# Performance work log

Hardware: AMD Instinct MI355X
Metric: run time of the kernel (lower is better)

The kernel has to match this reference:

```python
import jax, jax.numpy as jnp
import numpy as np

B, T, D, H, NL = 8, 1024, 512, 8, 3
WS = (3, 5, 7)


def _mha(q_in, k_in, v_in, wq, bq, wk, bk, wv, bv, wo, bo):
    """Faithful copy of the torch MultiHeadAttention, including the
    transpose-free .view(B*H, -1, dh) head split (row-major reshape)."""
    bs = q_in.shape[0]
    dh = D // H
    q = (q_in @ wq + bq).reshape(bs * H, -1, dh)
    k = (k_in @ wk + bk).reshape(bs * H, -1, dh)
    v = (v_in @ wv + bv).reshape(bs * H, -1, dh)
    scores = jnp.einsum('bqd,bkd->bqk', q, k) / (dh ** 0.5)
    weights = jax.nn.softmax(scores, axis=-1)
    att = jnp.einsum('bqk,bkd->bqd', weights, v).reshape(bs, -1, D)
    return att @ wo + bo


def _forward(x, loc_wq, loc_bq, loc_wk, loc_bk, loc_wv, loc_bv, loc_wo, loc_bo,
             g_wq, g_bq, g_wk, g_bk, g_wv, g_bv, g_wo, g_bo, out_w, out_b):
    feats = []
    for lv in range(NL):
        w = WS[lv]
        pad = (w - 1) // 2
        xp = jnp.pad(x, ((0, 0), (pad, pad), (0, 0)))  # [B, T+2p, D]
        idx = jnp.arange(T)[:, None] + jnp.arange(w)[None, :]  # [T, w]
        win = xp[:, idx, :].reshape(B * T, w, D)  # sliding windows, same as unfold+permute
        lo = _mha(win, win, win,
                  loc_wq[lv], loc_bq[lv], loc_wk[lv], loc_bk[lv],
                  loc_wv[lv], loc_bv[lv], loc_wo[lv], loc_bo[lv])
        feats.append(lo.reshape(B, T, w, D).mean(axis=2))
    feats.append(_mha(x, x, x, g_wq, g_bq, g_wk, g_bk, g_wv, g_bv, g_wo, g_bo))
    combined = jnp.concatenate(feats, axis=-1)  # [B, T, D*(NL+1)]
    return combined @ out_w + out_b  # dropout is identity in eval mode


def setup_inputs() -> dict:
    key = jax.random.key(0)
    ks = jax.random.split(key, 20)
    s = 0.02
    d = {}
    d['x'] = jax.random.normal(ks[0], (B, T, D), jnp.float32)
    d['loc_wq'] = jax.random.normal(ks[1], (NL, D, D), jnp.float32) * s
    d['loc_bq'] = jax.random.normal(ks[2], (NL, D), jnp.float32) * s
    d['loc_wk'] = jax.random.normal(ks[3], (NL, D, D), jnp.float32) * s
    d['loc_bk'] = jax.random.normal(ks[4], (NL, D), jnp.float32) * s
    d['loc_wv'] = jax.random.normal(ks[5], (NL, D, D), jnp.float32) * s
    d['loc_bv'] = jax.random.normal(ks[6], (NL, D), jnp.float32) * s
    d['loc_wo'] = jax.random.normal(ks[7], (NL, D, D), jnp.float32) * s
    d['loc_bo'] = jax.random.normal(ks[8], (NL, D), jnp.float32) * s
    d['g_wq'] = jax.random.normal(ks[9], (D, D), jnp.float32) * s
    d['g_bq'] = jax.random.normal(ks[10], (D,), jnp.float32) * s
    d['g_wk'] = jax.random.normal(ks[11], (D, D), jnp.float32) * s
    d['g_bk'] = jax.random.normal(ks[12], (D,), jnp.float32) * s
    d['g_wv'] = jax.random.normal(ks[13], (D, D), jnp.float32) * s
    d['g_bv'] = jax.random.normal(ks[14], (D,), jnp.float32) * s
    d['g_wo'] = jax.random.normal(ks[15], (D, D), jnp.float32) * s
    d['g_bo'] = jax.random.normal(ks[16], (D,), jnp.float32) * s
    d['out_w'] = jax.random.normal(ks[17], (D * (NL + 1), D), jnp.float32) * s
    d['out_b'] = jax.random.normal(ks[18], (D,), jnp.float32) * s
    return d


def reference(x, loc_wq, loc_bq, loc_wk, loc_bk, loc_wv, loc_bv, loc_wo, loc_bo,
              g_wq, g_bq, g_wk, g_bk, g_wv, g_bv, g_wo, g_bo, out_w, out_b):
    return _forward(x, loc_wq, loc_bq, loc_wk, loc_bk, loc_wv, loc_bv, loc_wo, loc_bo,
                    g_wq, g_bq, g_wk, g_bk, g_wv, g_bv, g_wo, g_bo, out_w, out_b)
```

## Files before the change

kernel.cpp:

```cpp
#include <hip/hip_runtime.h>
#include <hip/hip_bf16.h>
#include <cstddef>

#define T_SEQ 1024
#define D_MODEL 512

typedef __attribute__((ext_vector_type(8))) __bf16 bf16x8;
typedef __attribute__((ext_vector_type(4))) float f32x4;
typedef __attribute__((ext_vector_type(16))) float f32x16;
typedef __attribute__((ext_vector_type(8))) unsigned short u16x8;
typedef __attribute__((ext_vector_type(4))) unsigned int u32x4;

typedef const unsigned int __attribute__((address_space(1)))* gas1_t;
typedef unsigned int __attribute__((address_space(3)))* las3_t;

__device__ __forceinline__ void gload_lds16(const void* g, void* l) {
  __builtin_amdgcn_global_load_lds((gas1_t)g, (las3_t)l, 16, 0, 0);
}

__device__ __forceinline__ float bf2f(unsigned short u) {
  return __uint_as_float(((unsigned)u) << 16);
}
__device__ __forceinline__ unsigned short f2bf(float f) {
  __hip_bfloat16 h = __float2bfloat16(f);
// ... 31 lines not shown
    const int base = blockIdx.x * 16384 + t * 8;
#pragma unroll
    for (int it = 0; it < 8; ++it) {
      const int i = base + it * 2048;
      const float4 a = *(const float4*)(x + i);
      const float4 b = *(const float4*)(x + i + 4);
      u16x8 o;
      o[0] = f2bf(a.x); o[1] = f2bf(a.y); o[2] = f2bf(a.z); o[3] = f2bf(a.w);
      o[4] = f2bf(b.x); o[5] = f2bf(b.y); o[6] = f2bf(b.z); o[7] = f2bf(b.w);
      *(u16x8*)(xb + i) = o;
    }
    return;
  }
  if (z == 21) {
    const int i = blockIdx.x * 256 + t;
    if (blockIdx.x < 18) {
      const int which = i >> 9, lv = which / 3, role = which % 3, e = i & 511;
      const float* src = role == 0 ? loc_bq : role == 1 ? loc_bk : loc_bv;
      bqkvb[i] = __float2bfloat16(src[lv * 512 + e]);
    }
    return;
  }

  const float* src;
  bool tr = true;
  if (z < 3)       src = loc_wq + (size_t)z * MS;
  else if (z < 6)  src = loc_wk + (size_t)(z - 3) * MS;
  else if (z < 9)  src = loc_wv + (size_t)(z - 6) * MS;
  else if (z == 9)  src = g_wq;
  else if (z == 10) src = g_wk;
  else if (z == 11) src = g_wv;
  else if (z < 16) src = out_w + (size_t)(z - 12) * MS;
  else if (z < 19) { src = loc_wo + (size_t)(z - 16) * MS; tr = false; }
  else             { src = g_wo; tr = false; }
  __hip_bfloat16* dst = WT + (size_t)z * MS;

  const int tk = (blockIdx.x & 15) * 32;
  const int tn = (blockIdx.x >> 4) * 32;
  const int r = t >> 3, c4 = (t & 7) * 4;
  const float4 v = *(const float4*)(src + (size_t)(tk + r) * 512 + tn + c4);
  if (tr) {
    tile[r][c4 + 0] = v.x; tile[r][c4 + 1] = v.y;
    tile[r][c4 + 2] = v.z; tile[r][c4 + 3] = v.w;
    __syncthreads();
    ushort4 o;
    o.x = f2bf(tile[c4 + 0][r]); o.y = f2bf(tile[c4 + 1][r]);
    o.z = f2bf(tile[c4 + 2][r]); o.w = f2bf(tile[c4 + 3][r]);
    *(ushort4*)(dst + (size_t)(tn + r) * 512 + tk + c4) = o;
  } else {
    ushort4 o;
    o.x = f2bf(v.x); o.y = f2bf(v.y); o.z = f2bf(v.z); o.w = f2bf(v.w);
    *(ushort4*)(dst + (size_t)(tk + r) * 512 + tn + c4) = o;
  }
}

__global__ __launch_bounds__(256)
void bias_fuse_kernel(const float* __restrict__ loc_bo, const float* __restrict__ g_bo,
                      const float* __restrict__ out_w, const float* __restrict__ out_b,
                      float* __restrict__ bfused) {
  const int z = blockIdx.y;
  const int n = blockIdx.x * 256 + threadIdx.x;
  const float* bo = (z < 3) ? loc_bo + z * 512 : g_bo;
  const float* W = out_w + (size_t)z * 512 * 512;
  float acc = (z == 0) ? out_b[n] : 0.f;
  for (int m = 0; m < 512; ++m)
    acc = fmaf(bo[m], W[(size_t)m * 512 + n], acc);
  bfused[z * 512 + n] = acc;
}

__device__ __forceinline__ void gemm_core_b128(
    const __hip_bfloat16* __restrict__ A, const __hip_bfloat16* __restrict__ BT,
    __hip_bfloat16* As, __hip_bfloat16* Bs, int row0, int col0, f32x4 acc[4][4]) {
  const int tid = threadIdx.x;
  const int wv = tid >> 6, lane = tid & 63;
  const int g = lane >> 4, r16 = lane & 15;
  const int wm = wv >> 1, wn = wv & 1;
  const char* Ab = (const char*)A;
  const char* Bb = (const char*)BT;
  for (int k0 = 0; k0 < 512; k0 += 32) {
    {
      const int row = tid >> 2, off = (tid & 3) << 4;
      gload_lds16(Ab + (size_t)(row0 + row) * 1024 + k0 * 2 + off,
                  (char*)As + (wv << 10));
      const int i2 = tid + 256;
      const int row2 = i2 >> 2, off2 = (i2 & 3) << 4;
      gload_lds16(Ab + (size_t)(row0 + row2) * 1024 + k0 * 2 + off2,
                  (char*)As + 4096 + (wv << 10));
    }
    {
      const int row = tid >> 2, off = (tid & 3) << 4;
      gload_lds16(Bb + (size_t)(col0 + row) * 1024 + k0 * 2 + off,
                  (char*)Bs + (wv << 10));
      const int i2 = tid + 256;
      const int row2 = i2 >> 2, off2 = (i2 & 3) << 4;
      gload_lds16(Bb + (size_t)(col0 + row2) * 1024 + k0 * 2 + off2,
                  (char*)Bs + 4096 + (wv << 10));
    }
    __syncthreads();
    bf16x8 a[4], b[4];
#pragma unroll
    for (int m = 0; m < 4; ++m)
      a[m] = *(const bf16x8*)(As + (wm * 64 + m * 16 + r16) * 32 + g * 8);
#pragma unroll
    for (int n = 0; n < 4; ++n)
      b[n] = *(const bf16x8*)(Bs + (wn * 64 + n * 16 + r16) * 32 + g * 8);
#pragma unroll
    for (int m = 0; m < 4; ++m)
#pragma unroll
      for (int n = 0; n < 4; ++n)
        acc[m][n] = __builtin_amdgcn_mfma_f32_16x16x32_bf16(a[m], b[n], acc[m][n], 0, 0, 0);
    __syncthreads();
  }
}

__device__ __forceinline__ void gemm_core_b64(
    const __hip_bfloat16* __restrict__ A, const __hip_bfloat16* __restrict__ BT,
    __hip_bfloat16* As, __hip_bfloat16* Bs, int row0, int col0, f32x4 acc[2][4]) {
  const int tid = threadIdx.x;
  const int wv = tid >> 6, lane = tid & 63;
  const int g = lane >> 4, r16 = lane & 15;
  const int wm = wv >> 1, wn = wv & 1;
  const char* Ab = (const char*)A;
  const char* Bb = (const char*)BT;
  for (int k0 = 0; k0 < 512; k0 += 32) {
    {
      const int row = tid >> 2, off = (tid & 3) << 4;
      gload_lds16(Ab + (size_t)(row0 + row) * 1024 + k0 * 2 + off,
                  (char*)As + (wv << 10));
    }
    {
      const int row = tid >> 2, off = (tid & 3) << 4;
      gload_lds16(Bb + (size_t)(col0 + row) * 1024 + k0 * 2 + off,
                  (char*)Bs + (wv << 10));
      const int i2 = tid + 256;
      const int row2 = i2 >> 2, off2 = (i2 & 3) << 4;
      gload_lds16(Bb + (size_t)(col0 + row2) * 1024 + k0 * 2 + off2,
                  (char*)Bs + 4096 + (wv << 10));
    }
    __syncthreads();
    bf16x8 a[2], b[4];
#pragma unroll
    for (int m = 0; m < 2; ++m)
      a[m] = *(const bf16x8*)(As + (wm * 32 + m * 16 + r16) * 32 + g * 8);
#pragma unroll
    for (int n = 0; n < 4; ++n)
      b[n] = *(const bf16x8*)(Bs + (wn * 64 + n * 16 + r16) * 32 + g * 8);
#pragma unroll
    for (int m = 0; m < 2; ++m)
#pragma unroll
      for (int n = 0; n < 4; ++n)
        acc[m][n] = __builtin_amdgcn_mfma_f32_16x16x32_bf16(a[m], b[n], acc[m][n], 0, 0, 0);
    __syncthreads();
  }
}

__global__ __launch_bounds__(256)
void gemm_qkv_kernel(const __hip_bfloat16* __restrict__ A,
                     const __hip_bfloat16* __restrict__ WT_base, size_t wt_stride,
                     const float* __restrict__ b0, const float* __restrict__ b1,
                     const float* __restrict__ b2,
                     __hip_bfloat16* __restrict__ out_base) {
  __shared__ __attribute__((aligned(16))) __hip_bfloat16 As[4096];
  __shared__ __attribute__((aligned(16))) __hip_bfloat16 Bs[4096];
  const int z = blockIdx.z;
  const __hip_bfloat16* WT = WT_base + (size_t)z * wt_stride;
  const float* bias = (z == 0) ? b0 : (z == 1) ? b1 : b2;
  __hip_bfloat16* C = out_base + (size_t)z * (size_t)(8192 * 512);
  const int row0 = blockIdx.y * 128, col0 = blockIdx.x * 128;
  f32x4 acc[4][4];
#pragma unroll
  for (int m = 0; m < 4; ++m)
#pragma unroll
    for (int n = 0; n < 4; ++n) acc[m][n] = (f32x4)(0.0f);
  gemm_core_b128(A, WT, As, Bs, row0, col0, acc);
  const int lane = threadIdx.x & 63, wv = threadIdx.x >> 6;
  const int g = lane >> 4, r16 = lane & 15, wm = wv >> 1, wn = wv & 1;
#pragma unroll
  for (int n = 0; n < 4; ++n) {
    const int col = col0 + wn * 64 + n * 16 + r16;
    const float bn = bias[col];
#pragma unroll
    for (int m = 0; m < 4; ++m) {
      const int rowb = row0 + wm * 64 + m * 16 + g * 4;
#pragma unroll
      for (int r = 0; r < 4; ++r)
        C[(size_t)(rowb + r) * 512 + col] = __float2bfloat16(acc[m][n][r] + bn);
    }
  }
}

__global__ __launch_bounds__(256)
void gemm_fusew_kernel(const __hip_bfloat16* __restrict__ A_base,
                       const __hip_bfloat16* __restrict__ BT_base,
                       __hip_bfloat16* __restrict__ C_base) {
  __shared__ __attribute__((aligned(16))) __hip_bfloat16 As[4096];
  __shared__ __attribute__((aligned(16))) __hip_bfloat16 Bs[4096];
  const size_t MS = (size_t)512 * 512;
  const int z = blockIdx.z;
  const __hip_bfloat16* A = A_base + z * MS;
  const __hip_bfloat16* BT = BT_base + z * MS;
  __hip_bfloat16* C = C_base + z * MS;
  const int row0 = blockIdx.y * 128, col0 = blockIdx.x * 128;
  f32x4 acc[4][4];
#pragma unroll
  for (int m = 0; m < 4; ++m)
#pragma unroll
    for (int n = 0; n < 4; ++n) acc[m][n] = (f32x4)(0.0f);
  gemm_core_b128(A, BT, As, Bs, row0, col0, acc);
  const int lane = threadIdx.x & 63, wv = threadIdx.x >> 6;
  const int g = lane >> 4, r16 = lane & 15, wm = wv >> 1, wn = wv & 1;
#pragma unroll
  for (int n = 0; n < 4; ++n) {
    const int col = col0 + wn * 64 + n * 16 + r16;
#pragma unroll
    for (int m = 0; m < 4; ++m) {
      const int rowb = row0 + wm * 64 + m * 16 + g * 4;
#pragma unroll
      for (int r = 0; r < 4; ++r)
        C[(size_t)(rowb + r) * 512 + col] = __float2bfloat16(acc[m][n][r]);
    }
  }
}

__global__ __launch_bounds__(256)
void gemm_out_fused_kernel(const __hip_bfloat16* __restrict__ A0,
                           const __hip_bfloat16* __restrict__ A1,
                           const __hip_bfloat16* __restrict__ A2,
                           const __hip_bfloat16* __restrict__ A3,
                           const __hip_bfloat16* __restrict__ WT_base,
                           const float* __restrict__ bfused,
                           float* __restrict__ out) {
  __shared__ __attribute__((aligned(16))) __hip_bfloat16 As[2048];
  __shared__ __attribute__((aligned(16))) __hip_bfloat16 Bs[4096];
  const size_t MS = (size_t)512 * 512;
  const int row0 = blockIdx.y * 64, col0 = blockIdx.x * 128;
  f32x4 acc[2][4];
#pragma unroll
  for (int m = 0; m < 2; ++m)
#pragma unroll
    for (int n = 0; n < 4; ++n) acc[m][n] = (f32x4)(0.0f);
  const __hip_bfloat16* Az[4] = {A0, A1, A2, A3};
  for (int z = 0; z < 4; ++z)
    gemm_core_b64(Az[z], WT_base + (size_t)z * MS, As, Bs, row0, col0, acc);
  const int lane = threadIdx.x & 63, wv = threadIdx.x >> 6;
  const int g = lane >> 4, r16 = lane & 15, wm = wv >> 1, wn = wv & 1;
#pragma unroll
  for (int n = 0; n < 4; ++n) {
    const int col = col0 + wn * 64 + n * 16 + r16;
    const float bn = bfused[col] + bfused[512 + col] + bfused[1024 + col] +
                     bfused[1536 + col];
#pragma unroll
    for (int m = 0; m < 2; ++m) {
      const int rowb = row0 + wm * 32 + m * 16 + g * 4;
#pragma unroll
      for (int r = 0; r < 4; ++r)
        out[(size_t)(rowb + r) * 512 + col] = acc[m][n][r] + bn;
    }
  }
}

template <int W>
__device__ __forceinline__ const __hip_bfloat16* slot_row(
    const __hip_bfloat16* __restrict__ X, const __hip_bfloat16* __restrict__ biasb,
    int b, int tloc, int pg, int sl, int* ch_out) {
  constexpr int PAD = (W - 1) / 2;
  const int hloc = sl >> 3, p = sl & 7;
  const int m = (pg * 4 + hloc) * W + p;
  const int j = m >> 3;
  *ch_out = m & 7;
  int sr = tloc + j - PAD;
  if (p < W) {
    if (sr >= 0 && sr < T_SEQ) return X + ((size_t)(b * T_SEQ + sr) << 9);
    return biasb;
  }
  sr = sr < 0 ? 0 : (sr > T_SEQ - 1 ? T_SEQ - 1 : sr);
  return X + ((size_t)(b * T_SEQ + sr) << 9);
}

template <int W>
__global__ __launch_bounds__(256)
void local_attn_mfma_kernel(const __hip_bfloat16* __restrict__ Xq,
                            const __hip_bfloat16* __restrict__ Xk,
                            const __hip_bfloat16* __restrict__ Xv,
                            const __hip_bfloat16* __restrict__ bqb,
                            const __hip_bfloat16* __restrict__ bkb,
                            const __hip_bfloat16* __restrict__ bvb,
                            __hip_bfloat16* __restrict__ abar) {
  __shared__ unsigned lds_u[4][2048];
  const int tid = threadIdx.x;
  const int wv = tid >> 6, lane = tid & 63;
  const int bt = blockIdx.x * 4 + wv;
  const int b = bt >> 10, tloc = bt & 1023;
  unsigned* L = &lds_u[wv][0];
  const int dl = lane & 31, hi = lane >> 5;

  {
    const int k2 = dl, dhalf = hi;
    int ch0, ch1;
    const __hip_bfloat16* r0 =
        slot_row<W>(Xv, bvb, b, tloc, (2 * k2) >> 5, (2 * k2) & 31, &ch0);
    const __hip_bfloat16* r1 =
        slot_row<W>(Xv, bvb, b, tloc, (2 * k2 + 1) >> 5, (2 * k2 + 1) & 31, &ch1);
    u16x8 A0[4], A1[4];
#pragma unroll
    for (int q = 0; q < 4; ++q) {
      A0[q] = *(const u16x8*)(r0 + ch0 * 64 + dhalf * 32 + q * 8);
      A1[q] = *(const u16x8*)(r1 + ch1 * 64 + dhalf * 32 + q * 8);
    }
#pragma unroll
    for (int q = 0; q < 4; ++q)
#pragma unroll
      for (int e = 0; e < 8; ++e) {
        const int d_ = dhalf * 32 + q * 8 + e;
        const unsigned dw = (unsigned)A0[q][e] | ((unsigned)A1[q][e] << 16);
        const int byte = (d_ * 128 + k2 * 4) ^ ((d_ & 7) << 4);
        L[byte >> 2] = dw;
      }
  }

  f32x16 accP[2][2];
#pragma unroll
  for (int pg = 0; pg < 2; ++pg)
#pragma unroll
    for (int dh = 0; dh < 2; ++dh) accP[pg][dh] = (f32x16)(0.0f);

  const int myb = dl >> 3;

#pragma unroll
  for (int pg = 0; pg < 2; ++pg) {
    int chK, chQ;
    const __hip_bfloat16* rK = slot_row<W>(Xk, bkb, b, tloc, pg, dl, &chK);
    const __hip_bfloat16* rQ = slot_row<W>(Xq, bqb, b, tloc, pg, dl, &chQ);
    f32x16 sa = (f32x16)(0.0f);
#pragma unroll
    for (int i = 0; i < 4; ++i) {
      const bf16x8 kf = *(const bf16x8*)(rK + chK * 64 + i * 16 + hi * 8);
      const bf16x8 qf = *(const bf16x8*)(rQ + chQ * 64 + i * 16 + hi * 8);
      sa = __builtin_amdgcn_mfma_f32_32x32x16_bf16(kf, qf, sa, 0, 0, 0);
    }

    float sel[4];
#pragma unroll
    for (int r4 = 0; r4 < 4; ++r4)
      sel[r4] = (myb == 0) ? sa[r4]
              : (myb == 1) ? sa[4 + r4]
              : (myb == 2) ? sa[8 + r4] : sa[12 + r4];
// ... 30 lines not shown
      for (int dh = 0; dh < 2; ++dh) {
        const int d_ = dh * 32 + dl;
        const int off = (d_ * 128 + pg * 64 + kh * 32 + hi * 16) ^ ((d_ & 7) << 4);
        const bf16x8 va =
            __builtin_bit_cast(bf16x8, *(const u32x4*)((const char*)L + off));
        accP[pg][dh] = __builtin_amdgcn_mfma_f32_32x32x16_bf16(va, pf, accP[pg][dh], 0, 0, 0);
      }
    }
  }

#pragma unroll
  for (int pg = 0; pg < 2; ++pg) {
    if ((dl & 7) < W) {
      const int m_o = (pg * 4 + (dl >> 3)) * W + (dl & 7);
#pragma unroll
      for (int dh = 0; dh < 2; ++dh) {
#pragma unroll
        for (int rq = 0; rq < 4; ++rq) {
          unsigned wa, wb;
          CVTPK(wa, accP[pg][dh][4 * rq + 0], accP[pg][dh][4 * rq + 1]);
          CVTPK(wb, accP[pg][dh][4 * rq + 2], accP[pg][dh][4 * rq + 3]);
          const int dwi = m_o * 34 + dh * 16 + rq * 4 + hi * 2;
          uint2 w; w.x = wa; w.y = wb;
          *(uint2*)(L + dwi) = w;
        }
      }
    }
  }
  asm volatile("s_waitcnt lgkmcnt(0)" ::: "memory");

  const int cho = lane >> 3, fb = lane & 7;
  float o[8] = {0.f, 0.f, 0.f, 0.f, 0.f, 0.f, 0.f, 0.f};
#pragma unroll
  for (int jj = 0; jj < W; ++jj) {
    const int mo = 8 * jj + cho;
    const uint2 w0 = *(const uint2*)(L + mo * 34 + fb * 4);
    const uint2 w1 = *(const uint2*)(L + mo * 34 + fb * 4 + 2);
    o[0] += bf2f((unsigned short)(w0.x & 0xffff));
    o[1] += bf2f((unsigned short)(w0.x >> 16));
    o[2] += bf2f((unsigned short)(w0.y & 0xffff));
    o[3] += bf2f((unsigned short)(w0.y >> 16));
    o[4] += bf2f((unsigned short)(w1.x & 0xffff));
    o[5] += bf2f((unsigned short)(w1.x >> 16));
    o[6] += bf2f((unsigned short)(w1.y & 0xffff));
    o[7] += bf2f((unsigned short)(w1.y >> 16));
  }
  const float invw = 1.f / (float)W;
  u16x8 ov;
#pragma unroll
  for (int e2 = 0; e2 < 8; ++e2) ov[e2] = f2bf(o[e2] * invw);
  *(u16x8*)(abar + ((size_t)bt << 9) + cho * 64 + fb * 8) = ov;
}

__global__ __launch_bounds__(256)
void global_attn_mfma_kernel(const __hip_bfloat16* __restrict__ Xq,
                             const __hip_bfloat16* __restrict__ Xk,
                             const __hip_bfloat16* __restrict__ Xv,
                             __hip_bfloat16* __restrict__ att) {
  __shared__ unsigned vt[2][2048];
  const int tid = threadIdx.x;
  const int lane = tid & 63;
  const int wv = tid >> 6;
  const int qblk = blockIdx.x;
  const int bh = blockIdx.y;
  const size_t base = (size_t)bh << 16;
  const int c = lane & 31;
  const int g = lane >> 5;
  const int q0 = qblk * 128 + wv * 32;

  const __hip_bfloat16* Qp = Xq + base;
  const __hip_bfloat16* Kp = Xk + base;
  const __hip_bfloat16* Vp = Xv + base;

  bf16x8 qf[4];
#pragma unroll
  for (int s = 0; s < 4; ++s)
    qf[s] = *(const bf16x8*)(Qp + (size_t)(q0 + c) * 64 + s * 16 + g * 8);

  const int k2 = tid & 31, dblk = tid >> 5;

  bf16x8 kf[2][4];
  u16x8 v0, v1, v0n, v1n;

  v0 = *(const u16x8*)(Vp + (size_t)(2 * k2) * 64 + dblk * 8);
  v1 = *(const u16x8*)(Vp + (size_t)(2 * k2 + 1) * 64 + dblk * 8);
#pragma unroll
  for (int kb = 0; kb < 2; ++kb)
#pragma unroll
    for (int s = 0; s < 4; ++s)
      kf[kb][s] = *(const bf16x8*)(Kp + (size_t)(kb * 32 + c) * 64 + s * 16 + g * 8);

  f32x16 Oa = (f32x16)(0.0f), Ob = (f32x16)(0.0f);
  float m_run = -3e38f, l_run = 0.f;

  for (int kt = 0; kt < 16; ++kt) {
    unsigned* vb = &vt[kt & 1][0];
#pragma unroll
    for (int jj = 0; jj < 8; ++jj) {
      const int d = dblk * 8 + jj;
      const unsigned dw = (unsigned)v0[jj] | ((unsigned)v1[jj] << 16);
      const int byte = (d * 128 + k2 * 4) ^ ((d & 7) << 4);
      vb[byte >> 2] = dw;
    }
    if (kt < 15) {
      const __hip_bfloat16* vsrc = Vp + (size_t)((kt + 1) * 64 + 2 * k2) * 64 + dblk * 8;
      v0n = *(const u16x8*)vsrc;
      v1n = *(const u16x8*)(vsrc + 64);
    }
    __syncthreads();

    f32x16 sa = (f32x16)(0.0f), sb = (f32x16)(0.0f);
#pragma unroll
    for (int s = 0; s < 4; ++s)
      sa = __builtin_amdgcn_mfma_f32_32x32x16_bf16(kf[0][s], qf[s], sa, 0, 0, 0);
#pragma unroll
    for (int s = 0; s < 4; ++s)
      sb = __builtin_amdgcn_mfma_f32_32x32x16_bf16(kf[1][s], qf[s], sb, 0, 0, 0);

    if (kt < 15) {
#pragma unroll
      for (int kb = 0; kb < 2; ++kb)
#pragma unroll
        for (int s = 0; s < 4; ++s)
          kf[kb][s] = *(const bf16x8*)(Kp + (size_t)((kt + 1) * 64 + kb * 32 + c) * 64 +
                                       s * 16 + g * 8);
    }

    float mx = sa[0];
#pragma unroll
    for (int r = 1; r < 16; ++r) mx = fmaxf(mx, sa[r]);
#pragma unroll
    for (int r = 0; r < 16; ++r) mx = fmaxf(mx, sb[r]);
    mx = fmaxf(mx, __shfl_xor(mx, 32));
    const float m_new = fmaxf(m_run, mx * 0.125f);
    const float alpha = __expf(m_run - m_new);

    float p0[16], p1[16];
    float lsum = 0.f;
#pragma unroll
    for (int r = 0; r < 16; ++r) { p0[r] = __expf(fmaf(sa[r], 0.125f, -m_new)); lsum += p0[r]; }
#pragma unroll
    for (int r = 0; r < 16; ++r) { p1[r] = __expf(fmaf(sb[r], 0.125f, -m_new)); lsum += p1[r]; }
    lsum += __shfl_xor(lsum, 32);
    l_run = fmaf(l_run, alpha, lsum);
    m_run = m_new;
#pragma unroll
    for (int r = 0; r < 16; ++r) { Oa[r] *= alpha; Ob[r] *= alpha; }

    unsigned bw[2][2][4];
#define REDIST(pb, kb_)                                                  \
    {                                                                    \
      unsigned t0_, t1_, t2_, t3_, t4_, t5_, t6_, t7_;                   \
      CVTPK(t0_, pb[0], pb[1]);   CVTPK(t1_, pb[2], pb[3]);              \
      CVTPK(t2_, pb[4], pb[5]);   CVTPK(t3_, pb[6], pb[7]);              \
      CVTPK(t4_, pb[8], pb[9]);   CVTPK(t5_, pb[10], pb[11]);            \
      CVTPK(t6_, pb[12], pb[13]); CVTPK(t7_, pb[14], pb[15]);            \
      swap32(t0_, t2_, lane); swap32(t1_, t3_, lane);                    \
      swap32(t4_, t6_, lane); swap32(t5_, t7_, lane);                    \
      bw[kb_][0][0] = t0_; bw[kb_][0][1] = t1_; bw[kb_][0][2] = t2_;     \
      bw[kb_][0][3] = t3_;                                               \
      bw[kb_][1][0] = t4_; bw[kb_][1][1] = t5_; bw[kb_][1][2] = t6_;     \
      bw[kb_][1][3] = t7_;                                               \
    }
    REDIST(p0, 0)
    REDIST(p1, 1)
#undef REDIST

    const unsigned* vbr = &vt[kt & 1][0];
#pragma unroll
    for (int kb = 0; kb < 2; ++kb)
#pragma unroll
      for (int st = 0; st < 2; ++st) {
        const u32x4 pw = { bw[kb][st][0], bw[kb][st][1], bw[kb][st][2], bw[kb][st][3] };
        const bf16x8 pf = __builtin_bit_cast(bf16x8, pw);
        {
          const int row = c;
          const int off = (row * 128 + (kb * 64 + st * 32 + g * 16)) ^ ((row & 7) << 4);
          const bf16x8 va = __builtin_bit_cast(bf16x8, *(const u32x4*)((const char*)vbr + off));
          Oa = __builtin_amdgcn_mfma_f32_32x32x16_bf16(va, pf, Oa, 0, 0, 0);
        }
        {
          const int row = 32 + c;
          const int off = (row * 128 + (kb * 64 + st * 32 + g * 16)) ^ ((row & 7) << 4);
          const bf16x8 va = __builtin_bit_cast(bf16x8, *(const u32x4*)((const char*)vbr + off));
          Ob = __builtin_amdgcn_mfma_f32_32x32x16_bf16(va, pf, Ob, 0, 0, 0);
        }
      }

    v0 = v0n; v1 = v1n;
  }

  const float inv = 1.f / l_run;
  __hip_bfloat16* drow = att + base + (size_t)(q0 + c) * 64;
#pragma unroll
  for (int qd = 0; qd < 4; ++qd) {
    unsigned lo, hi2;
    {
      const float a0 = Oa[4 * qd + 0] * inv, a1 = Oa[4 * qd + 1] * inv;
      const float a2 = Oa[4 * qd + 2] * inv, a3 = Oa[4 * qd + 3] * inv;
      CVTPK(lo, a0, a1); CVTPK(hi2, a2, a3);
      uint2 w; w.x = lo; w.y = hi2;
      *(uint2*)(drow + 8 * qd + 4 * g) = w;
    }
    {
      const float a0 = Ob[4 * qd + 0] * inv, a1 = Ob[4 * qd + 1] * inv;
      const float a2 = Ob[4 * qd + 2] * inv, a3 = Ob[4 * qd + 3] * inv;
      CVTPK(lo, a0, a1); CVTPK(hi2, a2, a3);
      uint2 w; w.x = lo; w.y = hi2;
      *(uint2*)(drow + 32 + 8 * qd + 4 * g) = w;
    }
  }
}

extern "C" void kernel_launch(void* const* d_in, const int* in_sizes, int n_in,
                              void* d_out, int out_size, void* d_ws, size_t ws_size,
                              hipStream_t stream) {
  const float* x      = (const float*)d_in[0];
  const float* loc_wq = (const float*)d_in[1];
  const float* loc_bq = (const float*)d_in[2];
  const float* loc_wk = (const float*)d_in[3];
  const float* loc_bk = (const float*)d_in[4];
  const float* loc_wv = (const float*)d_in[5];
  const float* loc_bv = (const float*)d_in[6];
  const float* loc_wo = (const float*)d_in[7];
  const float* loc_bo = (const float*)d_in[8];
  const float* g_wq  = (const float*)d_in[9];
  const float* g_bq  = (const float*)d_in[10];
  const float* g_wk  = (const float*)d_in[11];
  const float* g_bk  = (const float*)d_in[12];
  const float* g_wv  = (const float*)d_in[13];
  const float* g_bv  = (const float*)d_in[14];
  const float* g_wo  = (const float*)d_in[15];
  const float* g_bo  = (const float*)d_in[16];
  const float* out_w = (const float*)d_in[17];
  const float* out_b = (const float*)d_in[18];
  float* out = (float*)d_out;

  __hip_bfloat16* wsb = (__hip_bfloat16*)d_ws;
  const size_t SZ = (size_t)8192 * 512;
  const size_t MS = (size_t)512 * 512;
  __hip_bfloat16* xb    = wsb;
  __hip_bfloat16* WT    = wsb + SZ;
  __hip_bfloat16* Xq    = wsb + SZ + 24 * MS;
  __hip_bfloat16* Xk    = Xq + SZ;
  __hip_bfloat16* Xv    = Xq + 2 * SZ;
  __hip_bfloat16* abar0 = Xq + 3 * SZ;
  __hip_bfloat16* abar1 = Xq + 4 * SZ;
  __hip_bfloat16* abar2 = Xq + 5 * SZ;
  __hip_bfloat16* abar3 = Xq + 6 * SZ;
  float* bfused = (float*)(Xq + 7 * SZ);
  __hip_bfloat16* bqkvb = (__hip_bfloat16*)(bfused + 2048);
  __hip_bfloat16* abars[3] = {abar0, abar1, abar2};

  const dim3 thr(256);

  prep_weights_kernel<<<dim3(256, 22), thr, 0, stream>>>(
      loc_wq, loc_wk, loc_wv, g_wq, g_wk, g_wv, out_w, loc_wo, g_wo,
      x, loc_bq, loc_bk, loc_bv, WT, xb, bqkvb);
  gemm_fusew_kernel<<<dim3(4, 4, 4), thr, 0, stream>>>(WT + 12 * MS, WT + 16 * MS,
                                                       WT + 20 * MS);
  bias_fuse_kernel<<<dim3(2, 4), thr, 0, stream>>>(loc_bo, g_bo, out_w, out_b, bfused);

  const dim3 gqkv(4, 64, 3);

  for (int lv = 0; lv < 3; ++lv) {
    gemm_qkv_kernel<<<gqkv, thr, 0, stream>>>(
        xb, WT + lv * MS, 3 * MS,
        loc_bq + lv * 512, loc_bk + lv * 512, loc_bv + lv * 512, Xq);

    const __hip_bfloat16* bqb = bqkvb + (lv * 3 + 0) * 512;
    const __hip_bfloat16* bkb = bqkvb + (lv * 3 + 1) * 512;
    const __hip_bfloat16* bvb = bqkvb + (lv * 3 + 2) * 512;
    if (lv == 0)
      local_attn_mfma_kernel<3><<<2048, thr, 0, stream>>>(Xq, Xk, Xv, bqb, bkb, bvb, abars[lv]);
    else if (lv == 1)
      local_attn_mfma_kernel<5><<<2048, thr, 0, stream>>>(Xq, Xk, Xv, bqb, bkb, bvb, abars[lv]);
    else
      local_attn_mfma_kernel<7><<<2048, thr, 0, stream>>>(Xq, Xk, Xv, bqb, bkb, bvb, abars[lv]);
  }

  gemm_qkv_kernel<<<gqkv, thr, 0, stream>>>(xb, WT + 9 * MS, MS, g_bq, g_bk, g_bv, Xq);
  global_attn_mfma_kernel<<<dim3(8, 64), thr, 0, stream>>>(Xq, Xk, Xv, abar3);

  gemm_out_fused_kernel<<<dim3(4, 128), thr, 0, stream>>>(abar0, abar1, abar2, abar3,
                                                          WT + 20 * MS, bfused, out);
}
```

Measured before the change: 290.1 us.

## Merge all QKV projections and attention levels into two persistent mega-kernels

When workspace allows, all twelve QKV projection GEMMs plus the weight-fusion GEMM and bias fusion run as one launch, and all three local-window attentions plus global attention run as a second single launch. This replaces about ten serialized launches, each with low occupancy tails, with two wide grids so independent work can overlap across CUs. It costs much more workspace to hold every projection at once, and falls back to the old sequence when the workspace is too small.

```diff
diff --git a/kernel.cpp b/kernel.cpp
--- a/kernel.cpp
+++ b/kernel.cpp
@@ -107,20 +107,6 @@
     o.x = f2bf(v.x); o.y = f2bf(v.y); o.z = f2bf(v.z); o.w = f2bf(v.w);
     *(ushort4*)(dst + (size_t)(tk + r) * 512 + tn + c4) = o;
   }
-}
-
-__global__ __launch_bounds__(256)
-void bias_fuse_kernel(const float* __restrict__ loc_bo, const float* __restrict__ g_bo,
-                      const float* __restrict__ out_w, const float* __restrict__ out_b,
-                      float* __restrict__ bfused) {
-  const int z = blockIdx.y;
-  const int n = blockIdx.x * 256 + threadIdx.x;
-  const float* bo = (z < 3) ? loc_bo + z * 512 : g_bo;
-  const float* W = out_w + (size_t)z * 512 * 512;
-  float acc = (z == 0) ? out_b[n] : 0.f;
-  for (int m = 0; m < 512; ++m)
-    acc = fmaf(bo[m], W[(size_t)m * 512 + n], acc);
-  bfused[z * 512 + n] = acc;
 }
 
 __device__ __forceinline__ void gemm_core_b128(
@@ -209,19 +195,10 @@
   }
 }
 
-__global__ __launch_bounds__(256)
-void gemm_qkv_kernel(const __hip_bfloat16* __restrict__ A,
-                     const __hip_bfloat16* __restrict__ WT_base, size_t wt_stride,
-                     const float* __restrict__ b0, const float* __restrict__ b1,
-                     const float* __restrict__ b2,
-                     __hip_bfloat16* __restrict__ out_base) {
-  __shared__ __attribute__((aligned(16))) __hip_bfloat16 As[4096];
-  __shared__ __attribute__((aligned(16))) __hip_bfloat16 Bs[4096];
-  const int z = blockIdx.z;
-  const __hip_bfloat16* WT = WT_base + (size_t)z * wt_stride;
-  const float* bias = (z == 0) ? b0 : (z == 1) ? b1 : b2;
-  __hip_bfloat16* C = out_base + (size_t)z * (size_t)(8192 * 512);
-  const int row0 = blockIdx.y * 128, col0 = blockIdx.x * 128;
+__device__ __forceinline__ void gemm_bias_body(
+    const __hip_bfloat16* __restrict__ A, const __hip_bfloat16* __restrict__ WT,
+    const float* __restrict__ bias, __hip_bfloat16* __restrict__ C,
+    int row0, int col0, __hip_bfloat16* As, __hip_bfloat16* Bs) {
   f32x4 acc[4][4];
 #pragma unroll
   for (int m = 0; m < 4; ++m)
@@ -233,7 +210,7 @@
 #pragma unroll
   for (int n = 0; n < 4; ++n) {
     const int col = col0 + wn * 64 + n * 16 + r16;
-    const float bn = bias[col];
+    const float bn = bias ? bias[col] : 0.f;
 #pragma unroll
     for (int m = 0; m < 4; ++m) {
       const int rowb = row0 + wm * 64 + m * 16 + g * 4;
@@ -244,73 +221,73 @@
   }
 }
 
+__device__ __forceinline__ void bias_fuse_body(
+    const float* __restrict__ bo, const float* __restrict__ W,
+    const float* __restrict__ add, float* __restrict__ bfz, int n) {
+  float acc = add ? add[n] : 0.f;
+  for (int m = 0; m < 512; ++m)
+    acc = fmaf(bo[m], W[(size_t)m * 512 + n], acc);
+  bfz[n] = acc;
+}
+
 __global__ __launch_bounds__(256)
-void gemm_fusew_kernel(const __hip_bfloat16* __restrict__ A_base,
-                       const __hip_bfloat16* __restrict__ BT_base,
-                       __hip_bfloat16* __restrict__ C_base) {
+void mega_gemm_kernel(const __hip_bfloat16* __restrict__ xb,
+                      const __hip_bfloat16* __restrict__ WT,
+                      const float* __restrict__ loc_bq, const float* __restrict__ loc_bk,
+                      const float* __restrict__ loc_bv, const float* __restrict__ g_bq,
+                      const float* __restrict__ g_bk, const float* __restrict__ g_bv,
+                      const float* __restrict__ loc_bo, const float* __restrict__ g_bo,
+                      const float* __restrict__ out_w, const float* __restrict__ out_b,
+                      __hip_bfloat16* __restrict__ proj, float* __restrict__ bfused) {
   __shared__ __attribute__((aligned(16))) __hip_bfloat16 As[4096];
   __shared__ __attribute__((aligned(16))) __hip_bfloat16 Bs[4096];
   const size_t MS = (size_t)512 * 512;
-  const int z = blockIdx.z;
-  const __hip_bfloat16* A = A_base + z * MS;
-  const __hip_bfloat16* BT = BT_base + z * MS;
-  __hip_bfloat16* C = C_base + z * MS;
-  const int row0 = blockIdx.y * 128, col0 = blockIdx.x * 128;
-  f32x4 acc[4][4];
-#pragma unroll
-  for (int m = 0; m < 4; ++m)
-#pragma unroll
-    for (int n = 0; n < 4; ++n) acc[m][n] = (f32x4)(0.0f);
-  gemm_core_b128(A, BT, As, Bs, row0, col0, acc);
-  const int lane = threadIdx.x & 63, wv = threadIdx.x >> 6;
-  const int g = lane >> 4, r16 = lane & 15, wm = wv >> 1, wn = wv & 1;
-#pragma unroll
-  for (int n = 0; n < 4; ++n) {
-    const int col = col0 + wn * 64 + n * 16 + r16;
-#pragma unroll
-    for (int m = 0; m < 4; ++m) {
-      const int rowb = row0 + wm * 64 + m * 16 + g * 4;
-#pragma unroll
-      for (int r = 0; r < 4; ++r)
-        C[(size_t)(rowb + r) * 512 + col] = __float2bfloat16(acc[m][n][r]);
-    }
-  }
-}
-
-__global__ __launch_bounds__(256)
-void gemm_out_fused_kernel(const __hip_bfloat16* __restrict__ A0,
-                           const __hip_bfloat16* __restrict__ A1,
-                           const __hip_bfloat16* __restrict__ A2,
-                           const __hip_bfloat16* __restrict__ A3,
-                           const __hip_bfloat16* __restrict__ WT_base,
-                           const float* __restrict__ bfused,
-                           float* __restrict__ out) {
-  __shared__ __attribute__((aligned(16))) __hip_bfloat16 As[2048];
-  __shared__ __attribute__((aligned(16))) __hip_bfloat16 Bs[4096];
-  const size_t MS = (size_t)512 * 512;
-  const int row0 = blockIdx.y * 64, col0 = blockIdx.x * 128;
-  f32x4 acc[2][4];
-#pragma unroll
-  for (int m = 0; m < 2; ++m)
-#pragma unroll
-    for (int n = 0; n < 4; ++n) acc[m][n] = (f32x4)(0.0f);
-  const __hip_bfloat16* Az[4] = {A0, A1, A2, A3};
-  for (int z = 0; z < 4; ++z)
-    gemm_core_b64(Az[z], WT_base + (size_t)z * MS, As, Bs, row0, col0, acc);
-  const int lane = threadIdx.x & 63, wv = threadIdx.x >> 6;
-  const int g = lane >> 4, r16 = lane & 15, wm = wv >> 1, wn = wv & 1;
-#pragma unroll
-  for (int n = 0; n < 4; ++n) {
-    const int col = col0 + wn * 64 + n * 16 + r16;
-    const float bn = bfused[col] + bfused[512 + col] + bfused[1024 + col] +
-                     bfused[1536 + col];
-#pragma unroll
-    for (int m = 0; m < 2; ++m) {
-      const int rowb = row0 + wm * 32 + m * 16 + g * 4;
-#pragma unroll
-      for (int r = 0; r < 4; ++r)
-        out[(size_t)(rowb + r) * 512 + col] = acc[m][n][r] + bn;
-    }
+  const size_t SZ = (size_t)8192 * 512;
+  const int bid = blockIdx.x;
+
+  if (bid < 3072) {
+    const int oid = (bid & 7) * 384 + (bid >> 3);
+    const int y = oid / 48;
+    const int rem = oid - y * 48;
+    const int z = rem >> 2, xcol = rem & 3;
+    const float* bias;
+    if (z < 3)       bias = loc_bq + z * 512;
+    else if (z < 6)  bias = loc_bk + (z - 3) * 512;
+    else if (z < 9)  bias = loc_bv + (z - 6) * 512;
+    else             bias = (z == 9) ? g_bq : (z == 10) ? g_bk : g_bv;
+    gemm_bias_body(xb, WT + (size_t)z * MS, bias, proj + (size_t)z * SZ,
+                   y * 128, xcol * 128, As, Bs);
+  } else if (bid < 3136) {
+    const int i = bid - 3072;
+    const int z = i >> 4, y = (i >> 2) & 3, xcol = i & 3;
+    f32x4 acc[4][4];
+#pragma unroll
+    for (int m = 0; m < 4; ++m)
+#pragma unroll
+      for (int n = 0; n < 4; ++n) acc[m][n] = (f32x4)(0.0f);
+    gemm_core_b128(WT + (size_t)(12 + z) * MS, WT + (size_t)(16 + z) * MS,
+                   As, Bs, y * 128, xcol * 128, acc);
+    __hip_bfloat16* C = (__hip_bfloat16*)(WT + (size_t)(20 + z) * MS);
+    const int lane = threadIdx.x & 63, wv = threadIdx.x >> 6;
+    const int g = lane >> 4, r16 = lane & 15, wm = wv >> 1, wn = wv & 1;
+#pragma unroll
+    for (int n = 0; n < 4; ++n) {
+      const int col = xcol * 128 + wn * 64 + n * 16 + r16;
+#pragma unroll
+      for (int m = 0; m < 4; ++m) {
+        const int rowb = y * 128 + wm * 64 + m * 16 + g * 4;
+#pragma unroll
+        for (int r = 0; r < 4; ++r)
+          C[(size_t)(rowb + r) * 512 + col] = __float2bfloat16(acc[m][n][r]);
+      }
+    }
+  } else {
+    const int i = bid - 3136;
+    const int z = i >> 1;
+    const int n = (i & 1) * 256 + threadIdx.x;
+    const float* bo = (z < 3) ? loc_bo + z * 512 : g_bo;
+    bias_fuse_body(bo, out_w + (size_t)z * MS, z == 0 ? out_b : nullptr,
+                   bfused + z * 512, n);
   }
 }
 
@@ -333,20 +310,16 @@
 }
 
 template <int W>
-__global__ __launch_bounds__(256)
-void local_attn_mfma_kernel(const __hip_bfloat16* __restrict__ Xq,
-                            const __hip_bfloat16* __restrict__ Xk,
-                            const __hip_bfloat16* __restrict__ Xv,
-                            const __hip_bfloat16* __restrict__ bqb,
-                            const __hip_bfloat16* __restrict__ bkb,
-                            const __hip_bfloat16* __restrict__ bvb,
-                            __hip_bfloat16* __restrict__ abar) {
-  __shared__ unsigned lds_u[4][2048];
+__device__ __forceinline__ void local_attn_body(
+    int bx, const __hip_bfloat16* __restrict__ Xq, const __hip_bfloat16* __restrict__ Xk,
+    const __hip_bfloat16* __restrict__ Xv, const __hip_bfloat16* __restrict__ bqb,
+    const __hip_bfloat16* __restrict__ bkb, const __hip_bfloat16* __restrict__ bvb,
+    __hip_bfloat16* __restrict__ abar, unsigned* pool) {
   const int tid = threadIdx.x;
   const int wv = tid >> 6, lane = tid & 63;
-  const int bt = blockIdx.x * 4 + wv;
+  const int bt = bx * 4 + wv;
   const int b = bt >> 10, tloc = bt & 1023;
-  unsigned* L = &lds_u[wv][0];
+  unsigned* L = pool + wv * 2048;
   const int dl = lane & 31, hi = lane >> 5;
 
   {
@@ -483,102 +456,6 @@
   *(u16x8*)(abar + ((size_t)bt << 9) + cho * 64 + fb * 8) = ov;
 }
 
-__global__ __launch_bounds__(256)
-void global_attn_mfma_kernel(const __hip_bfloat16* __restrict__ Xq,
-                             const __hip_bfloat16* __restrict__ Xk,
-                             const __hip_bfloat16* __restrict__ Xv,
-                             __hip_bfloat16* __restrict__ att) {
-  __shared__ unsigned vt[2][2048];
-  const int tid = threadIdx.x;
-  const int lane = tid & 63;
-  const int wv = tid >> 6;
-  const int qblk = blockIdx.x;
-  const int bh = blockIdx.y;
-  const size_t base = (size_t)bh << 16;
-  const int c = lane & 31;
-  const int g = lane >> 5;
-  const int q0 = qblk * 128 + wv * 32;
-
-  const __hip_bfloat16* Qp = Xq + base;
-  const __hip_bfloat16* Kp = Xk + base;
-  const __hip_bfloat16* Vp = Xv + base;
-
-  bf16x8 qf[4];
-#pragma unroll
-  for (int s = 0; s < 4; ++s)
-    qf[s] = *(const bf16x8*)(Qp + (size_t)(q0 + c) * 64 + s * 16 + g * 8);
-
-  const int k2 = tid & 31, dblk = tid >> 5;
-
-  bf16x8 kf[2][4];
-  u16x8 v0, v1, v0n, v1n;
-
-  v0 = *(const u16x8*)(Vp + (size_t)(2 * k2) * 64 + dblk * 8);
-  v1 = *(const u16x8*)(Vp + (size_t)(2 * k2 + 1) * 64 + dblk * 8);
-#pragma unroll
-  for (int kb = 0; kb < 2; ++kb)
-#pragma unroll
-    for (int s = 0; s < 4; ++s)
-      kf[kb][s] = *(const bf16x8*)(Kp + (size_t)(kb * 32 + c) * 64 + s * 16 + g * 8);
-
-  f32x16 Oa = (f32x16)(0.0f), Ob = (f32x16)(0.0f);
-  float m_run = -3e38f, l_run = 0.f;
-
-  for (int kt = 0; kt < 16; ++kt) {
-    unsigned* vb = &vt[kt & 1][0];
-#pragma unroll
-    for (int jj = 0; jj < 8; ++jj) {
-      const int d = dblk * 8 + jj;
-      const unsigned dw = (unsigned)v0[jj] | ((unsigned)v1[jj] << 16);
-      const int byte = (d * 128 + k2 * 4) ^ ((d & 7) << 4);
-      vb[byte >> 2] = dw;
-    }
-    if (kt < 15) {
-      const __hip_bfloat16* vsrc = Vp + (size_t)((kt + 1) * 64 + 2 * k2) * 64 + dblk * 8;
-      v0n = *(const u16x8*)vsrc;
-      v1n = *(const u16x8*)(vsrc + 64);
-    }
-    __syncthreads();
-
-    f32x16 sa = (f32x16)(0.0f), sb = (f32x16)(0.0f);
-#pragma unroll
-    for (int s = 0; s < 4; ++s)
-      sa = __builtin_amdgcn_mfma_f32_32x32x16_bf16(kf[0][s], qf[s], sa, 0, 0, 0);
-#pragma unroll
-    for (int s = 0; s < 4; ++s)
-      sb = __builtin_amdgcn_mfma_f32_32x32x16_bf16(kf[1][s], qf[s], sb, 0, 0, 0);
-
-    if (kt < 15) {
-#pragma unroll
-      for (int kb = 0; kb < 2; ++kb)
-#pragma unroll
-        for (int s = 0; s < 4; ++s)
-          kf[kb][s] = *(const bf16x8*)(Kp + (size_t)((kt + 1) * 64 + kb * 32 + c) * 64 +
-                                       s * 16 + g * 8);
-    }
-
-    float mx = sa[0];
-#pragma unroll
-    for (int r = 1; r < 16; ++r) mx = fmaxf(mx, sa[r]);
-#pragma unroll
-    for (int r = 0; r < 16; ++r) mx = fmaxf(mx, sb[r]);
-    mx = fmaxf(mx, __shfl_xor(mx, 32));
-    const float m_new = fmaxf(m_run, mx * 0.125f);
-    const float alpha = __expf(m_run - m_new);
-
-    float p0[16], p1[16];
-    float lsum = 0.f;
-#pragma unroll
-    for (int r = 0; r < 16; ++r) { p0[r] = __expf(fmaf(sa[r], 0.125f, -m_new)); lsum += p0[r]; }
-#pragma unroll
-    for (int r = 0; r < 16; ++r) { p1[r] = __expf(fmaf(sb[r], 0.125f, -m_new)); lsum += p1[r]; }
-    lsum += __shfl_xor(lsum, 32);
-    l_run = fmaf(l_run, alpha, lsum);
-    m_run = m_new;
-#pragma unroll
-    for (int r = 0; r < 16; ++r) { Oa[r] *= alpha; Ob[r] *= alpha; }
-
-    unsigned bw[2][2][4];
 #define REDIST(pb, kb_)                                                  \
     {                                                                    \
       unsigned t0_, t1_, t2_, t3_, t4_, t5_, t6_, t7_;                   \
@@ -593,11 +470,103 @@
       bw[kb_][1][0] = t4_; bw[kb_][1][1] = t5_; bw[kb_][1][2] = t6_;     \
       bw[kb_][1][3] = t7_;                                               \
     }
+
+__device__ __forceinline__ void global_attn_body(
+    int qblk, int bh, const __hip_bfloat16* __restrict__ Xq,
+    const __hip_bfloat16* __restrict__ Xk, const __hip_bfloat16* __restrict__ Xv,
+    __hip_bfloat16* __restrict__ att, unsigned* pool) {
+  const int tid = threadIdx.x;
+  const int lane = tid & 63;
+  const int wv = tid >> 6;
+  const size_t base = (size_t)bh << 16;
+  const int c = lane & 31;
+  const int g = lane >> 5;
+  const int q0 = qblk * 128 + wv * 32;
+
+  const __hip_bfloat16* Qp = Xq + base;
+  const __hip_bfloat16* Kp = Xk + base;
+  const __hip_bfloat16* Vp = Xv + base;
+
+  bf16x8 qf[4];
+#pragma unroll
+  for (int s = 0; s < 4; ++s)
+    qf[s] = *(const bf16x8*)(Qp + (size_t)(q0 + c) * 64 + s * 16 + g * 8);
+
+  const int k2 = tid & 31, dblk = tid >> 5;
+
+  bf16x8 kf[2][4];
+  u16x8 v0, v1, v0n, v1n;
+
+  v0 = *(const u16x8*)(Vp + (size_t)(2 * k2) * 64 + dblk * 8);
+  v1 = *(const u16x8*)(Vp + (size_t)(2 * k2 + 1) * 64 + dblk * 8);
+#pragma unroll
+  for (int kb = 0; kb < 2; ++kb)
+#pragma unroll
+    for (int s = 0; s < 4; ++s)
+      kf[kb][s] = *(const bf16x8*)(Kp + (size_t)(kb * 32 + c) * 64 + s * 16 + g * 8);
+
+  f32x16 Oa = (f32x16)(0.0f), Ob = (f32x16)(0.0f);
+  float m_run = -3e38f, l_run = 0.f;
+
+  for (int kt = 0; kt < 16; ++kt) {
+    unsigned* vb = pool + (kt & 1) * 2048;
+#pragma unroll
+    for (int jj = 0; jj < 8; ++jj) {
+      const int d = dblk * 8 + jj;
+      const unsigned dw = (unsigned)v0[jj] | ((unsigned)v1[jj] << 16);
+      const int byte = (d * 128 + k2 * 4) ^ ((d & 7) << 4);
+      vb[byte >> 2] = dw;
+    }
+    if (kt < 15) {
+      const __hip_bfloat16* vsrc = Vp + (size_t)((kt + 1) * 64 + 2 * k2) * 64 + dblk * 8;
+      v0n = *(const u16x8*)vsrc;
+      v1n = *(const u16x8*)(vsrc + 64);
+    }
+    __syncthreads();
+
+    f32x16 sa = (f32x16)(0.0f), sb = (f32x16)(0.0f);
+#pragma unroll
+    for (int s = 0; s < 4; ++s)
+      sa = __builtin_amdgcn_mfma_f32_32x32x16_bf16(kf[0][s], qf[s], sa, 0, 0, 0);
+#pragma unroll
+    for (int s = 0; s < 4; ++s)
+      sb = __builtin_amdgcn_mfma_f32_32x32x16_bf16(kf[1][s], qf[s], sb, 0, 0, 0);
+
+    if (kt < 15) {
+#pragma unroll
+      for (int kb = 0; kb < 2; ++kb)
+#pragma unroll
+        for (int s = 0; s < 4; ++s)
+          kf[kb][s] = *(const bf16x8*)(Kp + (size_t)((kt + 1) * 64 + kb * 32 + c) * 64 +
+                                       s * 16 + g * 8);
+    }
+
+    float mx = sa[0];
+#pragma unroll
+    for (int r = 1; r < 16; ++r) mx = fmaxf(mx, sa[r]);
+#pragma unroll
+    for (int r = 0; r < 16; ++r) mx = fmaxf(mx, sb[r]);
+    mx = fmaxf(mx, __shfl_xor(mx, 32));
+    const float m_new = fmaxf(m_run, mx * 0.125f);
+    const float alpha = __expf(m_run - m_new);
+
+    float p0[16], p1[16];
+    float lsum = 0.f;
+#pragma unroll
+    for (int r = 0; r < 16; ++r) { p0[r] = __expf(fmaf(sa[r], 0.125f, -m_new)); lsum += p0[r]; }
+#pragma unroll
+    for (int r = 0; r < 16; ++r) { p1[r] = __expf(fmaf(sb[r], 0.125f, -m_new)); lsum += p1[r]; }
+    lsum += __shfl_xor(lsum, 32);
+    l_run = fmaf(l_run, alpha, lsum);
+    m_run = m_new;
+#pragma unroll
+    for (int r = 0; r < 16; ++r) { Oa[r] *= alpha; Ob[r] *= alpha; }
+
+    unsigned bw[2][2][4];
     REDIST(p0, 0)
     REDIST(p1, 1)
-#undef REDIST
-
-    const unsigned* vbr = &vt[kt & 1][0];
+
+    const unsigned* vbr = pool + (kt & 1) * 2048;
 #pragma unroll
     for (int kb = 0; kb < 2; ++kb)
 #pragma unroll
@@ -641,6 +610,149 @@
       *(uint2*)(drow + 32 + 8 * qd + 4 * g) = w;
     }
   }
+}
+
+__global__ __launch_bounds__(256)
+void attn_all_kernel(const __hip_bfloat16* __restrict__ proj,
+                     const __hip_bfloat16* __restrict__ bqkvb,
+                     __hip_bfloat16* __restrict__ abar0, __hip_bfloat16* __restrict__ abar1,
+                     __hip_bfloat16* __restrict__ abar2, __hip_bfloat16* __restrict__ abar3) {
+  __shared__ __attribute__((aligned(16))) unsigned pool[8192];
+  const size_t SZ = (size_t)8192 * 512;
+  const int bid = blockIdx.x;
+  if (bid < 512) {
+    global_attn_body(bid & 7, bid >> 3, proj + 9 * SZ, proj + 10 * SZ, proj + 11 * SZ,
+                     abar3, pool);
+  } else {
+    const int lb = bid - 512;
+    const int lv = lb >> 11;
+    const int bx = lb & 2047;
+    if (lv == 0)
+      local_attn_body<3>(bx, proj + 0 * SZ, proj + 3 * SZ, proj + 6 * SZ,
+                         bqkvb + 0 * 512, bqkvb + 1 * 512, bqkvb + 2 * 512, abar0, pool);
+    else if (lv == 1)
+      local_attn_body<5>(bx, proj + 1 * SZ, proj + 4 * SZ, proj + 7 * SZ,
+                         bqkvb + 3 * 512, bqkvb + 4 * 512, bqkvb + 5 * 512, abar1, pool);
+    else
+      local_attn_body<7>(bx, proj + 2 * SZ, proj + 5 * SZ, proj + 8 * SZ,
+                         bqkvb + 6 * 512, bqkvb + 7 * 512, bqkvb + 8 * 512, abar2, pool);
+  }
+}
+
+__global__ __launch_bounds__(256)
+void gemm_out_fused_kernel(const __hip_bfloat16* __restrict__ A0,
+                           const __hip_bfloat16* __restrict__ A1,
+                           const __hip_bfloat16* __restrict__ A2,
+                           const __hip_bfloat16* __restrict__ A3,
+                           const __hip_bfloat16* __restrict__ WT_base,
+                           const float* __restrict__ bfused,
+                           float* __restrict__ out) {
+  __shared__ __attribute__((aligned(16))) __hip_bfloat16 As[2048];
+  __shared__ __attribute__((aligned(16))) __hip_bfloat16 Bs[4096];
+  const size_t MS = (size_t)512 * 512;
+  const int row0 = blockIdx.y * 64, col0 = blockIdx.x * 128;
+  f32x4 acc[2][4];
+#pragma unroll
+  for (int m = 0; m < 2; ++m)
+#pragma unroll
+    for (int n = 0; n < 4; ++n) acc[m][n] = (f32x4)(0.0f);
+  const __hip_bfloat16* Az[4] = {A0, A1, A2, A3};
+  for (int z = 0; z < 4; ++z)
+    gemm_core_b64(Az[z], WT_base + (size_t)z * MS, As, Bs, row0, col0, acc);
+  const int lane = threadIdx.x & 63, wv = threadIdx.x >> 6;
+  const int g = lane >> 4, r16 = lane & 15, wm = wv >> 1, wn = wv & 1;
+#pragma unroll
+  for (int n = 0; n < 4; ++n) {
+    const int col = col0 + wn * 64 + n * 16 + r16;
+    const float bn = bfused[col] + bfused[512 + col] + bfused[1024 + col] +
+                     bfused[1536 + col];
+#pragma unroll
+    for (int m = 0; m < 2; ++m) {
+      const int rowb = row0 + wm * 32 + m * 16 + g * 4;
+#pragma unroll
+      for (int r = 0; r < 4; ++r)
+        out[(size_t)(rowb + r) * 512 + col] = acc[m][n][r] + bn;
+    }
+  }
+}
+
+__global__ __launch_bounds__(256)
+void gemm_qkv_kernel(const __hip_bfloat16* __restrict__ A,
+                     const __hip_bfloat16* __restrict__ WT_base, size_t wt_stride,
+                     const float* __restrict__ b0, const float* __restrict__ b1,
+                     const float* __restrict__ b2,
+                     __hip_bfloat16* __restrict__ out_base) {
+  __shared__ __attribute__((aligned(16))) __hip_bfloat16 As[4096];
+  __shared__ __attribute__((aligned(16))) __hip_bfloat16 Bs[4096];
+  const int z = blockIdx.z;
+  const float* bias = (z == 0) ? b0 : (z == 1) ? b1 : b2;
+  gemm_bias_body(A, WT_base + (size_t)z * wt_stride, bias,
+                 out_base + (size_t)z * (size_t)(8192 * 512),
+                 blockIdx.y * 128, blockIdx.x * 128, As, Bs);
+}
+
+__global__ __launch_bounds__(256)
+void gemm_fusew_kernel(const __hip_bfloat16* __restrict__ A_base,
+                       const __hip_bfloat16* __restrict__ BT_base,
+                       __hip_bfloat16* __restrict__ C_base) {
+  __shared__ __attribute__((aligned(16))) __hip_bfloat16 As[4096];
+  __shared__ __attribute__((aligned(16))) __hip_bfloat16 Bs[4096];
+  const size_t MS = (size_t)512 * 512;
+  const int z = blockIdx.z;
+  f32x4 acc[4][4];
+#pragma unroll
+  for (int m = 0; m < 4; ++m)
+#pragma unroll
+    for (int n = 0; n < 4; ++n) acc[m][n] = (f32x4)(0.0f);
+  gemm_core_b128(A_base + z * MS, BT_base + z * MS, As, Bs,
+                 blockIdx.y * 128, blockIdx.x * 128, acc);
+  __hip_bfloat16* C = C_base + z * MS;
+  const int lane = threadIdx.x & 63, wv = threadIdx.x >> 6;
+  const int g = lane >> 4, r16 = lane & 15, wm = wv >> 1, wn = wv & 1;
+#pragma unroll
+  for (int n = 0; n < 4; ++n) {
+    const int col = blockIdx.x * 128 + wn * 64 + n * 16 + r16;
+#pragma unroll
+    for (int m = 0; m < 4; ++m) {
+      const int rowb = blockIdx.y * 128 + wm * 64 + m * 16 + g * 4;
+#pragma unroll
+      for (int r = 0; r < 4; ++r)
+        C[(size_t)(rowb + r) * 512 + col] = __float2bfloat16(acc[m][n][r]);
+    }
+  }
+}
+
+__global__ __launch_bounds__(256)
+void bias_fuse_kernel(const float* __restrict__ loc_bo, const float* __restrict__ g_bo,
+                      const float* __restrict__ out_w, const float* __restrict__ out_b,
+                      float* __restrict__ bfused) {
+  const int z = blockIdx.y;
+  const int n = blockIdx.x * 256 + threadIdx.x;
+  const float* bo = (z < 3) ? loc_bo + z * 512 : g_bo;
+  bias_fuse_body(bo, out_w + (size_t)z * 512 * 512, z == 0 ? out_b : nullptr,
+                 bfused + z * 512, n);
+}
+
+template <int W>
+__global__ __launch_bounds__(256)
+void local_attn_mfma_kernel(const __hip_bfloat16* __restrict__ Xq,
+                            const __hip_bfloat16* __restrict__ Xk,
+                            const __hip_bfloat16* __restrict__ Xv,
+                            const __hip_bfloat16* __restrict__ bqb,
+                            const __hip_bfloat16* __restrict__ bkb,
+                            const __hip_bfloat16* __restrict__ bvb,
+                            __hip_bfloat16* __restrict__ abar) {
+  __shared__ __attribute__((aligned(16))) unsigned pool[8192];
+  local_attn_body<W>(blockIdx.x, Xq, Xk, Xv, bqb, bkb, bvb, abar, pool);
+}
+
+__global__ __launch_bounds__(256)
+void global_attn_mfma_kernel(const __hip_bfloat16* __restrict__ Xq,
+                             const __hip_bfloat16* __restrict__ Xk,
+                             const __hip_bfloat16* __restrict__ Xv,
+                             __hip_bfloat16* __restrict__ att) {
+  __shared__ __attribute__((aligned(16))) unsigned pool[4096];
+  global_attn_body(blockIdx.x, blockIdx.y, Xq, Xk, Xv, att, pool);
 }
 
 extern "C" void kernel_launch(void* const* d_in, const int* in_sizes, int n_in,
@@ -670,48 +782,63 @@
   __hip_bfloat16* wsb = (__hip_bfloat16*)d_ws;
   const size_t SZ = (size_t)8192 * 512;
   const size_t MS = (size_t)512 * 512;
+
   __hip_bfloat16* xb    = wsb;
   __hip_bfloat16* WT    = wsb + SZ;
-  __hip_bfloat16* Xq    = wsb + SZ + 24 * MS;
-  __hip_bfloat16* Xk    = Xq + SZ;
-  __hip_bfloat16* Xv    = Xq + 2 * SZ;
-  __hip_bfloat16* abar0 = Xq + 3 * SZ;
-  __hip_bfloat16* abar1 = Xq + 4 * SZ;
-  __hip_bfloat16* abar2 = Xq + 5 * SZ;
-  __hip_bfloat16* abar3 = Xq + 6 * SZ;
-  float* bfused = (float*)(Xq + 7 * SZ);
-  __hip_bfloat16* bqkvb = (__hip_bfloat16*)(bfused + 2048);
-  __hip_bfloat16* abars[3] = {abar0, abar1, abar2};
+  float* bfused = (float*)(wsb + SZ + 24 * MS);
+  __hip_bfloat16* bqkvb = wsb + SZ + 24 * MS + 4096;
+  __hip_bfloat16* proj  = wsb + SZ + 24 * MS + 16384;
+
+  const size_t need_big = 2 * (17 * SZ + 24 * MS + 16384);
+  const bool big = ws_size >= need_big;
 
   const dim3 thr(256);
 
   prep_weights_kernel<<<dim3(256, 22), thr, 0, stream>>>(
       loc_wq, loc_wk, loc_wv, g_wq, g_wk, g_wv, out_w, loc_wo, g_wo,
       x, loc_bq, loc_bk, loc_bv, WT, xb, bqkvb);
-  gemm_fusew_kernel<<<dim3(4, 4, 4), thr, 0, stream>>>(WT + 12 * MS, WT + 16 * MS,
-                                                       WT + 20 * MS);
-  bias_fuse_kernel<<<dim3(2, 4), thr, 0, stream>>>(loc_bo, g_bo, out_w, out_b, bfused);
-
-  const dim3 gqkv(4, 64, 3);
-
-  for (int lv = 0; lv < 3; ++lv) {
-    gemm_qkv_kernel<<<gqkv, thr, 0, stream>>>(
-        xb, WT + lv * MS, 3 * MS,
-        loc_bq + lv * 512, loc_bk + lv * 512, loc_bv + lv * 512, Xq);
-
-    const __hip_bfloat16* bqb = bqkvb + (lv * 3 + 0) * 512;
-    const __hip_bfloat16* bkb = bqkvb + (lv * 3 + 1) * 512;
-    const __hip_bfloat16* bvb = bqkvb + (lv * 3 + 2) * 512;
-    if (lv == 0)
-      local_attn_mfma_kernel<3><<<2048, thr, 0, stream>>>(Xq, Xk, Xv, bqb, bkb, bvb, abars[lv]);
-    else if (lv == 1)
-      local_attn_mfma_kernel<5><<<2048, thr, 0, stream>>>(Xq, Xk, Xv, bqb, bkb, bvb, abars[lv]);
-    else
-      local_attn_mfma_kernel<7><<<2048, thr, 0, stream>>>(Xq, Xk, Xv, bqb, bkb, bvb, abars[lv]);
-  }
-
-  gemm_qkv_kernel<<<gqkv, thr, 0, stream>>>(xb, WT + 9 * MS, MS, g_bq, g_bk, g_bv, Xq);
-  global_attn_mfma_kernel<<<dim3(8, 64), thr, 0, stream>>>(Xq, Xk, Xv, abar3);
+
+  __hip_bfloat16 *abar0, *abar1, *abar2, *abar3;
+
+  if (big) {
+    abar0 = proj + 12 * SZ;
+    abar1 = proj + 13 * SZ;
+    abar2 = proj + 14 * SZ;
+    abar3 = proj + 15 * SZ;
+    mega_gemm_kernel<<<3144, thr, 0, stream>>>(
+        xb, WT, loc_bq, loc_bk, loc_bv, g_bq, g_bk, g_bv,
+        loc_bo, g_bo, out_w, out_b, proj, bfused);
+    attn_all_kernel<<<6656, thr, 0, stream>>>(proj, bqkvb, abar0, abar1, abar2, abar3);
+  } else {
+    gemm_fusew_kernel<<<dim3(4, 4, 4), thr, 0, stream>>>(WT + 12 * MS, WT + 16 * MS,
+                                                         WT + 20 * MS);
+    bias_fuse_kernel<<<dim3(2, 4), thr, 0, stream>>>(loc_bo, g_bo, out_w, out_b, bfused);
+    __hip_bfloat16* Xq = proj;
+    __hip_bfloat16* Xk = proj + SZ;
+    __hip_bfloat16* Xv = proj + 2 * SZ;
+    abar0 = proj + 3 * SZ;
+    abar1 = proj + 4 * SZ;
+    abar2 = proj + 5 * SZ;
+    abar3 = proj + 6 * SZ;
+    __hip_bfloat16* abars[3] = {abar0, abar1, abar2};
+    const dim3 gqkv(4, 64, 3);
+    for (int lv = 0; lv < 3; ++lv) {
+      gemm_qkv_kernel<<<gqkv, thr, 0, stream>>>(
+          xb, WT + lv * MS, 3 * MS,
+          loc_bq + lv * 512, loc_bk + lv * 512, loc_bv + lv * 512, Xq);
+      const __hip_bfloat16* bqb = bqkvb + (lv * 3 + 0) * 512;
+      const __hip_bfloat16* bkb = bqkvb + (lv * 3 + 1) * 512;
+      const __hip_bfloat16* bvb = bqkvb + (lv * 3 + 2) * 512;
+      if (lv == 0)
+        local_attn_mfma_kernel<3><<<2048, thr, 0, stream>>>(Xq, Xk, Xv, bqb, bkb, bvb, abars[lv]);
+      else if (lv == 1)
+        local_attn_mfma_kernel<5><<<2048, thr, 0, stream>>>(Xq, Xk, Xv, bqb, bkb, bvb, abars[lv]);
+      else
+        local_attn_mfma_kernel<7><<<2048, thr, 0, stream>>>(Xq, Xk, Xv, bqb, bkb, bvb, abars[lv]);
+    }
+    gemm_qkv_kernel<<<gqkv, thr, 0, stream>>>(xb, WT + 9 * MS, MS, g_bq, g_bk, g_bv, Xq);
+    global_attn_mfma_kernel<<<dim3(8, 64), thr, 0, stream>>>(Xq, Xk, Xv, abar3);
+  }
 
   gemm_out_fused_kernel<<<dim3(4, 128), thr, 0, stream>>>(abar0, abar1, abar2, abar3,
                                                           WT + 20 * MS, bfused, out);
```

Result: slower. 307.3 us (+5.9%).
